# Kernel optimization log

Measured on AMD Instinct MI355X. Metric: run time of the kernel, lower is better.

Reference implementation:

```python
import jax, jax.numpy as jnp
import numpy as np

B, C, H, W = 2, 128, 64, 64
D_STATE = 16
EXPAND = 2
D_INNER = C * EXPAND          # 256
DT_RANK = -(-C // 16)         # 8
K = 4                         # scan directions
COMPRESS = 3
SQUEEZE = 30
EPS = 1e-5


def layernorm(x, g, b):
    mu = x.mean(-1, keepdims=True)
    xm = x - mu
    var = (xm * xm).mean(-1, keepdims=True)
    return xm * jax.lax.rsqrt(var + EPS) * g + b


def conv2d(x, w, bias, pad):
    y = jax.lax.conv_general_dilated(x, w, (1, 1), ((pad, pad), (pad, pad)),
                                     dimension_numbers=('NCHW', 'OIHW', 'NCHW'))
    return y + bias[None, :, None, None]


def selective_scan(xs, dts, A, Bs, Cs):
    # xs,dts: (B,K,D,L); A: (K,D,N); Bs,Cs: (B,K,N,L)
    dt_t = jnp.moveaxis(dts, -1, 0)
    x_t = jnp.moveaxis(xs, -1, 0)
    B_t = jnp.moveaxis(Bs, -1, 0)
    C_t = jnp.moveaxis(Cs, -1, 0)
    h0 = jnp.zeros(xs.shape[:3] + (A.shape[-1],), xs.dtype)

    def step(h, inp):
        dt_l, x_l, b_l, c_l = inp          # (B,K,D),(B,K,D),(B,K,N),(B,K,N)
        dA = jnp.exp(dt_l[..., None] * A)  # (B,K,D,N)
        h = dA * h + (dt_l * x_l)[..., None] * b_l[:, :, None, :]
        y = jnp.einsum('bkdn,bkn->bkd', h, c_l)
        return h, y

    _, ys = jax.lax.scan(step, h0, (dt_t, x_t, B_t, C_t))
    return jnp.moveaxis(ys, 0, -1)  # (B,K,D,L)


def ss2d(x, p):  # x: (B,H,W,C) -> (B,H,W,C)
    xz = x @ p['in_proj_w'].T
    xc, z = jnp.split(xz, 2, axis=-1)
    xc = xc.transpose(0, 3, 1, 2)  # (B,D,H,W)
    xc = jax.lax.conv_general_dilated(xc, p['conv_w'], (1, 1), ((1, 1), (1, 1)),
                                      feature_group_count=D_INNER,
                                      dimension_numbers=('NCHW', 'OIHW', 'NCHW'))
    xc = jax.nn.silu(xc + p['conv_b'][None, :, None, None])
    b, d, h, w = xc.shape
    L = h * w
    x_hw = xc.reshape(b, d, L)
    x_wh = xc.transpose(0, 1, 3, 2).reshape(b, d, L)
    xs = jnp.stack([x_hw, x_wh, x_hw[..., ::-1], x_wh[..., ::-1]], axis=1)  # (B,4,D,L)
    x_dbl = jnp.einsum('bkdl,kcd->bkcl', xs, p['x_proj_w'])
    dtr, Bs, Cs = jnp.split(x_dbl, [DT_RANK, DT_RANK + D_STATE], axis=2)
    dts = jnp.einsum('bkrl,kdr->bkdl', dtr, p['dt_w'])
    dts = jax.nn.softplus(dts + p['dt_b'][None, :, :, None])
    A = -jnp.exp(p['A_logs']).reshape(K, d, D_STATE)
    ys = selective_scan(xs, dts, A, Bs, Cs)
    ys = ys + xs * p['Ds'].reshape(K, d)[None, :, :, None]
    inv = ys[:, 2:4][..., ::-1]  # undo flipped scans
    wh = lambda t: t.reshape(b, d, w, h).transpose(0, 1, 3, 2).reshape(b, d, L)
    y = ys[:, 0] + inv[:, 0] + wh(ys[:, 1]) + wh(inv[:, 1])
    y = y.transpose(0, 2, 1).reshape(b, h, w, d)
    y = layernorm(y, p['out_norm_g'], p['out_norm_b'])
    y = y * jax.nn.silu(z)
    return y @ p['out_proj_w'].T


def cab(x, p):  # x: (B,C,H,W)
    t = jax.nn.gelu(conv2d(x, p['cab_w1'], p['cab_b1'], 1), approximate=False)
    t = conv2d(t, p['cab_w2'], p['cab_b2'], 1)
    s = t.mean((2, 3), keepdims=True)
    s = jax.nn.relu(conv2d(s, p['ca_w1'], p['ca_b1'], 0))
    s = jax.nn.sigmoid(conv2d(s, p['ca_w2'], p['ca_b2'], 0))
    return t * s


def vss_block(input, p):
    inp = input.transpose(0, 2, 3, 1)  # (B,H,W,C)
    x = inp * p['skip_scale'] + ss2d(layernorm(inp, p['ln1_g'], p['ln1_b']), p)
    c = cab(layernorm(x, p['ln2_g'], p['ln2_b']).transpose(0, 3, 1, 2), p)
    x = x * p['skip_scale2'] + c.transpose(0, 2, 3, 1)
    return x.transpose(0, 3, 1, 2)


def setup_inputs() -> dict:
    key = jax.random.key(0)
    ks = jax.random.split(key, 16)
    rn = lambda i, shp, s=0.02: jax.random.normal(ks[i], shp, jnp.float32) * s
    return {
        'input': jax.random.normal(ks[0], (B, C, H, W), jnp.float32),
        'ln1_g': jnp.ones((C,), jnp.float32), 'ln1_b': jnp.zeros((C,), jnp.float32),
        'skip_scale': jnp.ones((C,), jnp.float32), 'skip_scale2': jnp.ones((C,), jnp.float32),
        'ln2_g': jnp.ones((C,), jnp.float32), 'ln2_b': jnp.zeros((C,), jnp.float32),
        'in_proj_w': rn(1, (2 * D_INNER, C)),
        'conv_w': rn(2, (D_INNER, 1, 3, 3), 0.1),
        'conv_b': jnp.zeros((D_INNER,), jnp.float32),
        'x_proj_w': rn(3, (K, DT_RANK + 2 * D_STATE, D_INNER)),
        'dt_w': rn(4, (K, D_INNER, DT_RANK), 0.1),
        'dt_b': rn(5, (K, D_INNER), 0.1),
        'A_logs': jnp.log(jnp.tile(jnp.arange(1, D_STATE + 1, dtype=jnp.float32), (K * D_INNER, 1))),
        'Ds': jnp.ones((K * D_INNER,), jnp.float32),
        'out_norm_g': jnp.ones((D_INNER,), jnp.float32), 'out_norm_b': jnp.zeros((D_INNER,), jnp.float32),
        'out_proj_w': rn(6, (C, D_INNER)),
        'cab_w1': rn(7, (C // COMPRESS, C, 3, 3), 0.05),
        'cab_b1': jnp.zeros((C // COMPRESS,), jnp.float32),
        'cab_w2': rn(8, (C, C // COMPRESS, 3, 3), 0.05),
        'cab_b2': jnp.zeros((C,), jnp.float32),
        'ca_w1': rn(9, (C // SQUEEZE, C, 1, 1), 0.05),
        'ca_b1': jnp.zeros((C // SQUEEZE,), jnp.float32),
        'ca_w2': rn(10, (C, C // SQUEEZE, 1, 1), 0.05),
        'ca_b2': jnp.zeros((C,), jnp.float32),
    }


def reference(input, ln1_g, ln1_b, skip_scale, skip_scale2, ln2_g, ln2_b,
              in_proj_w, conv_w, conv_b, x_proj_w, dt_w, dt_b, A_logs, Ds,
              out_norm_g, out_norm_b, out_proj_w,
              cab_w1, cab_b1, cab_w2, cab_b2, ca_w1, ca_b1, ca_w2, ca_b2):
    p = dict(ln1_g=ln1_g, ln1_b=ln1_b, skip_scale=skip_scale, skip_scale2=skip_scale2,
             ln2_g=ln2_g, ln2_b=ln2_b, in_proj_w=in_proj_w, conv_w=conv_w, conv_b=conv_b,
             x_proj_w=x_proj_w, dt_w=dt_w, dt_b=dt_b, A_logs=A_logs, Ds=Ds,
             out_norm_g=out_norm_g, out_norm_b=out_norm_b, out_proj_w=out_proj_w,
             cab_w1=cab_w1, cab_b1=cab_b1, cab_w2=cab_w2, cab_b2=cab_b2,
             ca_w1=ca_w1, ca_b1=ca_b1, ca_w2=ca_w2, ca_b2=ca_b2)
    return vss_block(input, p)
```

## Files before the change

kernel.cpp:

```cpp
#include <hip/hip_runtime.h>
#include <math.h>

#define BB 2
#define CC 128
#define HH 64
#define WW 64
#define LL 4096
#define DI 256
#define NS 16
#define KK 4
#define OC1 42

#define NC 256
#define CL 16

#define K3_POS 16
#define BCW 48

__device__ __forceinline__ float sigmoidf_(float x) { return 1.f / (1.f + __expf(-x)); }
__device__ __forceinline__ float siluf_(float x)    { return x * sigmoidf_(x); }

__device__ __forceinline__ int scan_pos(int k, int i) {
  if (k == 0) return i;
  if (k == 1) return ((i & 63) << 6) | (i >> 6);
  if (k == 2) return (LL - 1) - i;
  int j = (LL - 1) - i;
  return ((j & 63) << 6) | (j >> 6);
}

__global__ __launch_bounds__(256) void k1_ln_inproj(
    const float* __restrict__ inp, const float* __restrict__ g, const float* __restrict__ b,
    const float* __restrict__ wproj, float* __restrict__ xcin, float* __restrict__ zbuf) {
  __shared__ float sx[64][132];
  __shared__ float sw[128][68];
  __shared__ float smu[64], srs[64];
  const int tid = threadIdx.x;
  const int rt = blockIdx.x & 3;
  const int pt = blockIdx.x >> 2;
  const int bb = pt >> 6;
  const int pbase = (pt & 63) << 6;

  for (int idx = tid; idx < 64 * CC; idx += 256) {
    int c = idx >> 6, pl = idx & 63;
    sx[pl][c] = inp[((size_t)bb * CC + c) * LL + pbase + pl];
  }
  __syncthreads();
  {
    int pl = tid >> 2, j = tid & 3;
    float s = 0.f, s2 = 0.f;
    for (int c = j; c < CC; c += 4) { float v = sx[pl][c]; s += v; s2 += v * v; }
    s += __shfl_xor(s, 1); s2 += __shfl_xor(s2, 1);
    s += __shfl_xor(s, 2); s2 += __shfl_xor(s2, 2);
    if (j == 0) {
      float mu = s * (1.f / CC);
      smu[pl] = mu;
      srs[pl] = rsqrtf(s2 * (1.f / CC) - mu * mu + 1e-5f);
    }
  }
  __syncthreads();
  for (int idx = tid; idx < 64 * CC; idx += 256) {
    int c = idx & 127, pl = idx >> 7;
    sx[pl][c] = (sx[pl][c] - smu[pl]) * srs[pl] * g[c] + b[c];
  }

  const int pg = tid & 7, rg = tid >> 3;
  float acc[8][4];
#pragma unroll
  for (int j = 0; j < 8; j++)
#pragma unroll
    for (int q = 0; q < 4; q++) acc[j][q] = 0.f;

  for (int kc = 0; kc < CC; kc += 64) {
    __syncthreads();
    for (int idx = tid; idx < 128 * 64; idx += 256) {
      int cl = idx & 63, rl = idx >> 6;
      sw[rl][cl] = wproj[(size_t)(rt * 128 + rl) * CC + kc + cl];
    }
    __syncthreads();
#pragma unroll 4
    for (int i = 0; i < 16; i++) {
      const int k0 = kc + 4 * i, kl0 = 4 * i;
      float4 xv[8], wv[4];
#pragma unroll
      for (int j = 0; j < 8; j++) xv[j] = *(const float4*)&sx[pg + 8 * j][k0];
#pragma unroll
      for (int q = 0; q < 4; q++) wv[q] = *(const float4*)&sw[rg + 32 * q][kl0];
#pragma unroll
      for (int j = 0; j < 8; j++)
#pragma unroll
        for (int q = 0; q < 4; q++) {
          acc[j][q] += xv[j].x * wv[q].x + xv[j].y * wv[q].y
                     + xv[j].z * wv[q].z + xv[j].w * wv[q].w;
        }
    }
  }

  float* buf = (rt < 2) ? xcin : zbuf;
  const int drow = (rt & 1) * 128;
#pragma unroll
  for (int j = 0; j < 8; j++) {
    const int p = pbase + pg + 8 * j;
    float* dst = buf + ((size_t)bb * LL + p) * DI + drow;
#pragma unroll
    for (int q = 0; q < 4; q++) dst[rg + 32 * q] = acc[j][q];
  }
}

__global__ __launch_bounds__(256) void k2_dwconv(
    const float* __restrict__ xcin, const float* __restrict__ cw, const float* __restrict__ cb,
    float* __restrict__ xconv) {
  const int w0 = (blockIdx.x & 7) * 8;
  const int hh = (blockIdx.x >> 3) & 63;
  const int bb = blockIdx.x >> 9;
  const int d = threadIdx.x;

  float wv[9];
#pragma unroll
  for (int kk = 0; kk < 9; kk++) wv[kk] = cw[d * 9 + kk];
  const float bias = cb[d];

  float xin[3][10];
#pragma unroll
  for (int kh = 0; kh < 3; kh++) {
    int r = hh + kh - 1;
    bool vr = (r >= 0 && r < HH);
#pragma unroll
    for (int c = 0; c < 10; c++) {
      int cc2 = w0 + c - 1;
      bool vc = (cc2 >= 0 && cc2 < WW);
      xin[kh][c] = (vr && vc) ? xcin[((size_t)bb * LL + r * WW + cc2) * DI + d] : 0.f;
    }
  }
#pragma unroll
  for (int j = 0; j < 8; j++) {
    float acc = bias;
#pragma unroll
    for (int kh = 0; kh < 3; kh++)
#pragma unroll
      for (int kw = 0; kw < 3; kw++)
        acc += wv[kh * 3 + kw] * xin[kh][j + kw];
    xconv[((size_t)bb * LL + hh * WW + w0 + j) * DI + d] = siluf_(acc);
  }
}

__global__ __launch_bounds__(256) void k3_proj(
    const float* __restrict__ xconv, const float* __restrict__ xpw,
    float* __restrict__ BCbuf) {
  __shared__ float sx[16][68];
  __shared__ float sw[160][68];
  const int tid = threadIdx.x;
  const int bb = blockIdx.x >> 8;
  const int pbase = (blockIdx.x & 255) << 4;

  const int pg = tid & 7, rb = tid >> 3;
  float acc[2][5];
#pragma unroll
  for (int j = 0; j < 2; j++)
#pragma unroll
    for (int q = 0; q < 5; q++) acc[j][q] = 0.f;

  for (int kc = 0; kc < DI; kc += 64) {
    __syncthreads();
    for (int idx = tid; idx < 16 * 64; idx += 256) {
      int cl = idx & 63, pl = idx >> 6;
      sx[pl][cl] = xconv[((size_t)bb * LL + pbase + pl) * DI + kc + cl];
    }
    for (int idx = tid; idx < 160 * 64; idx += 256) {
      int cl = idx & 63, rl = idx >> 6;
      sw[rl][cl] = xpw[(size_t)rl * DI + kc + cl];
    }
    __syncthreads();
#pragma unroll 4
    for (int i = 0; i < 16; i++) {
      float4 xv[2], wv[5];
#pragma unroll
      for (int j = 0; j < 2; j++) xv[j] = *(const float4*)&sx[2 * pg + j][4 * i];
#pragma unroll
      for (int q = 0; q < 5; q++) wv[q] = *(const float4*)&sw[rb + 32 * q][4 * i];
#pragma unroll
      for (int j = 0; j < 2; j++)
#pragma unroll
        for (int q = 0; q < 5; q++) {
          acc[j][q] += xv[j].x * wv[q].x + xv[j].y * wv[q].y
                     + xv[j].z * wv[q].z + xv[j].w * wv[q].w;
        }
    }
  }

#pragma unroll
  for (int j = 0; j < 2; j++) {
    const int p = pbase + 2 * pg + j;
#pragma unroll
    for (int q = 0; q < 5; q++) {
      const int r = rb + 32 * q;
      const int k = r / 40, c0 = r - k * 40;
      BCbuf[((size_t)(bb * KK + k) * LL + p) * BCW + c0] = acc[j][q];
    }
  }
}

__global__ __launch_bounds__(256) void k4a_chunk(
    const float* __restrict__ xconv, const float* __restrict__ BCbuf,
    const float* __restrict__ A_logs, const float* __restrict__ dtw,
    const float* __restrict__ dtb,
    float* __restrict__ csS, float* __restrict__ csB) {
  __shared__ float sBC[CL][26];
  const int d = threadIdx.x;
  const int chunk = blockIdx.x & (NC - 1);
  const int t = blockIdx.x / NC;
  const int k = t & 3;
  const int bb = t >> 2;
  const int bk = bb * KK + k;
  const int base = chunk * CL;

  for (int idx = d; idx < CL * 24; idx += 256) {
    int ii = idx / 24, j = idx - ii * 24;
    int pos = scan_pos(k, base + ii);
    sBC[ii][j] = BCbuf[((size_t)bk * LL + pos) * BCW + j];
  }
  float a[NS];
  bool fast = true;
#pragma unroll
  for (int n = 0; n < NS; n++) {
    a[n] = -__expf(A_logs[((size_t)k * DI + d) * NS + n]);
    fast = fast && (fabsf(a[n] + (float)(n + 1)) < 1e-3f * (n + 1));
  }
  const float* wdt = dtw + ((size_t)k * DI + d) * 8;
  const float4 wd0 = *(const float4*)wdt;
  const float4 wd1 = *(const float4*)(wdt + 4);
  const float bdt = dtb[k * DI + d];
  __syncthreads();

  const float* x_p = xconv + (size_t)bb * LL * DI + d;

  float Bc[NS];
#pragma unroll
  for (int n = 0; n < NS; n++) Bc[n] = 0.f;
  float sumdt = 0.f;

  if (fast) {
#pragma unroll
    for (int half = 0; half < CL / 8; half++) {
      float xvr[8];
#pragma unroll
      for (int j = 0; j < 8; j++)
        xvr[j] = x_p[(size_t)scan_pos(k, base + half * 8 + j) * DI];
#pragma unroll
      for (int j = 0; j < 8; j++) {
        const int ii = half * 8 + j;
        const float* dr = sBC[ii];
        float u = bdt + wd0.x * dr[0] + wd0.y * dr[1] + wd0.z * dr[2] + wd0.w * dr[3]
                      + wd1.x * dr[4] + wd1.y * dr[5] + wd1.z * dr[6] + wd1.w * dr[7];
        float t2 = __expf(u);
        float E = __builtin_amdgcn_rcpf(1.f + t2);
        float dt = u > 20.f ? u : -0.69314718056f * __log2f(E);
        sumdt += dt;
        float dtx = dt * xvr[j];
        float E2 = E * E;
        float dA1 = E, dA2 = E2;
#pragma unroll
        for (int n = 0; n < NS; n += 2) {
          Bc[n] = dA1 * Bc[n] + dtx * sBC[ii][8 + n];
          Bc[n + 1] = dA2 * Bc[n + 1] + dtx * sBC[ii][9 + n];
          dA1 *= E2; dA2 *= E2;
        }
      }
    }
  } else {
#pragma unroll 2
    for (int ii = 0; ii < CL; ii++) {
      int pos = scan_pos(k, base + ii);
      float xv = x_p[(size_t)pos * DI];
      const float* dr = sBC[ii];
      float u = bdt + wd0.x * dr[0] + wd0.y * dr[1] + wd0.z * dr[2] + wd0.w * dr[3]
                    + wd1.x * dr[4] + wd1.y * dr[5] + wd1.z * dr[6] + wd1.w * dr[7];
      float t2 = __expf(u);
      float dt = u > 20.f ? u : log1pf(t2);
      sumdt += dt;
      float dtx = dt * xv;
#pragma unroll
      for (int n = 0; n < NS; n++) {
        float dA = __expf(dt * a[n]);
        Bc[n] = dA * Bc[n] + dtx * sBC[ii][8 + n];
      }
    }
  }
  csS[((size_t)bk * NC + chunk) * DI + d] = sumdt;
  size_t e = ((size_t)(bk * NC + chunk) * NS) * DI + d;
#pragma unroll
  for (int n = 0; n < NS; n++)
    csB[e + (size_t)n * DI] = Bc[n];
}

__global__ __launch_bounds__(256) void k4b_scanchunks(
    const float* __restrict__ csS, const float* __restrict__ csB,
    const float* __restrict__ A_logs, float* __restrict__ hin) {
  const int d = threadIdx.x;
  const int n = blockIdx.x & (NS - 1);
  const int bk = blockIdx.x >> 4;
  const int k = bk & 3;
  const float an = -__expf(A_logs[((size_t)k * DI + d) * NS + n]);
  const size_t strideB = (size_t)NS * DI;
  size_t e = ((size_t)bk * NC * NS + n) * DI + d;
  float H = 0.f;
  for (int c0 = 0; c0 < NC; c0 += 16) {
    float Ea[16], Bv[16];
#pragma unroll
    for (int j = 0; j < 16; j++) {
      Ea[j] = an * csS[((size_t)bk * NC + c0 + j) * DI + d];
      Bv[j] = csB[e + (size_t)j * strideB];
    }
#pragma unroll
    for (int j = 0; j < 16; j++) Ea[j] = __expf(Ea[j]);
#pragma unroll
    for (int j = 0; j < 16; j++) {
      hin[e + (size_t)j * strideB] = H;
      H = Ea[j] * H + Bv[j];
    }
    e += (size_t)16 * strideB;
  }
}

__global__ __launch_bounds__(256) void k4c_scan(
    const float* __restrict__ xconv, const float* __restrict__ BCbuf,
    const float* __restrict__ A_logs, const float* __restrict__ dtw,
    const float* __restrict__ dtb, const float* __restrict__ Ds,
    const float* __restrict__ hin, float* __restrict__ ys) {
  __shared__ float sBC[CL][BCW];
  const int d = threadIdx.x;
  const int chunk = blockIdx.x & (NC - 1);
  const int t = blockIdx.x / NC;
  const int k = t & 3;
  const int bb = t >> 2;
  const int bk = bb * KK + k;
  const int base = chunk * CL;

  for (int idx = d; idx < CL * 40; idx += 256) {
    int ii = idx / 40, j = idx - ii * 40;
    int pos = scan_pos(k, base + ii);
    sBC[ii][j] = BCbuf[((size_t)bk * LL + pos) * BCW + j];
  }
  float a[NS], h[NS];
  bool fast = true;
  const size_t eh = ((size_t)(bk * NC + chunk) * NS) * DI + d;
#pragma unroll
  for (int n = 0; n < NS; n++) {
    a[n] = -__expf(A_logs[((size_t)k * DI + d) * NS + n]);
    fast = fast && (fabsf(a[n] + (float)(n + 1)) < 1e-3f * (n + 1));
    h[n] = hin[eh + (size_t)n * DI];
  }
  const float* wdt = dtw + ((size_t)k * DI + d) * 8;
  const float4 wd0 = *(const float4*)wdt;
  const float4 wd1 = *(const float4*)(wdt + 4);
  const float bdt = dtb[k * DI + d];
  const float Dd = Ds[k * DI + d];
  __syncthreads();

  const float* x_p = xconv + (size_t)bb * LL * DI + d;
  float* ys_p = ys + (size_t)bk * LL * DI + d;

  if (fast) {
#pragma unroll
    for (int half = 0; half < CL / 8; half++) {
      float xvr[8];
#pragma unroll
      for (int j = 0; j < 8; j++)
        xvr[j] = x_p[(size_t)scan_pos(k, base + half * 8 + j) * DI];
#pragma unroll
      for (int j = 0; j < 8; j++) {
        const int ii = half * 8 + j;
        const float* dr = sBC[ii];
        float u = bdt + wd0.x * dr[0] + wd0.y * dr[1] + wd0.z * dr[2] + wd0.w * dr[3]
                      + wd1.x * dr[4] + wd1.y * dr[5] + wd1.z * dr[6] + wd1.w * dr[7];
        float t2 = __expf(u);
        float E = __builtin_amdgcn_rcpf(1.f + t2);
        float dt = u > 20.f ? u : -0.69314718056f * __log2f(E);
        float dtx = dt * xvr[j];
        float y = xvr[j] * Dd;
        float E2 = E * E;
        float dA1 = E, dA2 = E2;
#pragma unroll
        for (int n = 0; n < NS; n += 2) {
          h[n] = dA1 * h[n] + dtx * sBC[ii][8 + n];
          y += h[n] * sBC[ii][24 + n];
          h[n + 1] = dA2 * h[n + 1] + dtx * sBC[ii][9 + n];
          y += h[n + 1] * sBC[ii][25 + n];
          dA1 *= E2; dA2 *= E2;
        }
        ys_p[(size_t)scan_pos(k, base + ii) * DI] = y;
      }
    }
  } else {
#pragma unroll 2
    for (int ii = 0; ii < CL; ii++) {
      int pos = scan_pos(k, base + ii);
      float xv = x_p[(size_t)pos * DI];
      const float* dr = sBC[ii];
      float u = bdt + wd0.x * dr[0] + wd0.y * dr[1] + wd0.z * dr[2] + wd0.w * dr[3]
                    + wd1.x * dr[4] + wd1.y * dr[5] + wd1.z * dr[6] + wd1.w * dr[7];
      float t2 = __expf(u);
      float dt = u > 20.f ? u : log1pf(t2);
      float dtx = dt * xv;
      float y = xv * Dd;
#pragma unroll
      for (int n = 0; n < NS; n++) {
        float dA = __expf(dt * a[n]);
        h[n] = dA * h[n] + dtx * sBC[ii][8 + n];
        y += h[n] * sBC[ii][24 + n];
      }
      ys_p[(size_t)pos * DI] = y;
    }
  }
}

__global__ __launch_bounds__(256) void k5_fused(
    const float* __restrict__ ys, const float* __restrict__ zbuf,
    const float* __restrict__ ong, const float* __restrict__ onb,
    const float* __restrict__ opw,
    const float* __restrict__ inp, const float* __restrict__ sk,
    const float* __restrict__ g2, const float* __restrict__ b2,
    float* __restrict__ xresT, float* __restrict__ ln2) {
  __shared__ float sy[16][260];
  __shared__ float sw[128][68];
  __shared__ float sr[16][132];
  __shared__ float smu[16], srs[16];
  const int tid = threadIdx.x;
  const int bb = blockIdx.x >> 8;
  const int pbase = (blockIdx.x & 255) << 4;

  for (int idx = tid; idx < 16 * DI; idx += 256) {
    int d = idx & 255, pl = idx >> 8;
    size_t o0 = (((size_t)bb * KK + 0) * LL + pbase + pl) * DI + d;
    const size_t st = (size_t)LL * DI;
    sy[pl][d] = ys[o0] + ys[o0 + st] + ys[o0 + 2 * st] + ys[o0 + 3 * st];
  }
  __syncthreads();
  {
    int pl = tid >> 4, j = tid & 15;
    float s = 0.f, s2 = 0.f;
    for (int d = j; d < DI; d += 16) { float v = sy[pl][d]; s += v; s2 += v * v; }
#pragma unroll
    for (int m = 1; m < 16; m <<= 1) { s += __shfl_xor(s, m); s2 += __shfl_xor(s2, m); }
    if (j == 0) {
      float mu = s * (1.f / DI);
      smu[pl] = mu;
      srs[pl] = rsqrtf(s2 * (1.f / DI) - mu * mu + 1e-5f);
    }
  }
  __syncthreads();
  for (int idx = tid; idx < 16 * DI; idx += 256) {
    int d = idx & 255, pl = idx >> 8;
    float zv = zbuf[((size_t)bb * LL + pbase + pl) * DI + d];
    sy[pl][d] = ((sy[pl][d] - smu[pl]) * srs[pl] * ong[d] + onb[d]) * siluf_(zv);
  }

  const int pg = tid & 7, rb = tid >> 3;
  float acc[2][4];
#pragma unroll
  for (int j = 0; j < 2; j++)
#pragma unroll
    for (int q = 0; q < 4; q++) acc[j][q] = 0.f;

  for (int kc = 0; kc < DI; kc += 64) {
    __syncthreads();
    for (int idx = tid; idx < 128 * 64; idx += 256) {
      int cl = idx & 63, rl = idx >> 6;
      sw[rl][cl] = opw[(size_t)rl * DI + kc + cl];
    }
    __syncthreads();
#pragma unroll 4
    for (int i = 0; i < 16; i++) {
      float4 xv[2], wv[4];
#pragma unroll
      for (int j = 0; j < 2; j++) xv[j] = *(const float4*)&sy[2 * pg + j][kc + 4 * i];
#pragma unroll
      for (int q = 0; q < 4; q++) wv[q] = *(const float4*)&sw[rb + 32 * q][4 * i];
#pragma unroll
      for (int j = 0; j < 2; j++)
#pragma unroll
        for (int q = 0; q < 4; q++) {
          acc[j][q] += xv[j].x * wv[q].x + xv[j].y * wv[q].y
                     + xv[j].z * wv[q].z + xv[j].w * wv[q].w;
        }
    }
  }

#pragma unroll
  for (int j = 0; j < 2; j++) {
    const int p = pbase + 2 * pg + j;
#pragma unroll
    for (int q = 0; q < 4; q++) {
      const int c = rb + 32 * q;
      float r = inp[((size_t)bb * CC + c) * LL + p] * sk[c] + acc[j][q];
      sr[2 * pg + j][c] = r;
    }
  }
  __syncthreads();
  {
    int pl = tid >> 4, jj = tid & 15;
    float s = 0.f, s2 = 0.f;
    for (int c = jj; c < CC; c += 16) { float v = sr[pl][c]; s += v; s2 += v * v; }
#pragma unroll
    for (int m = 1; m < 16; m <<= 1) { s += __shfl_xor(s, m); s2 += __shfl_xor(s2, m); }
    if (jj == 0) {
      float mu = s * (1.f / CC);
      smu[pl] = mu;
      srs[pl] = rsqrtf(s2 * (1.f / CC) - mu * mu + 1e-5f);
    }
  }
  __syncthreads();
  for (int idx = tid; idx < 16 * CC; idx += 256) {
    int pl = idx & 15, c = idx >> 4;
    float r = sr[pl][c];
    size_t o = ((size_t)bb * CC + c) * LL + pbase + pl;
    xresT[o] = r;
    ln2[o] = (r - smu[pl]) * srs[pl] * g2[c] + b2[c];
  }
}

__global__ __launch_bounds__(256) void k6a_conv1(
    const float* __restrict__ ln2, const float* __restrict__ w1,
    float* __restrict__ pc1) {
  __shared__ float sIn[16][6][68];
  __shared__ float sw[16 * 9 * OC1];
  const int tid = threadIdx.x;
  const int icq = blockIdx.x & 7;
  const int h4  = (blockIdx.x >> 3) & 15;
  const int bb  = blockIdx.x >> 7;
  const int icb = icq * 16;

  for (int idx = tid; idx < 16 * 6 * 66; idx += 256) {
    int i = idx / 396, rem = idx % 396;
    int rr = rem / 66, j = rem % 66;
    int r = h4 * 4 + rr - 1, c2 = j - 1;
    float v = 0.f;
    if (r >= 0 && r < HH && c2 >= 0 && c2 < WW)
      v = ln2[((size_t)bb * CC + icb + i) * LL + r * WW + c2];
    sIn[i][rr][j] = v;
  }
  for (int idx = tid; idx < OC1 * 16 * 9; idx += 256) {
    int oc = idx / 144, rem = idx % 144;
    int i = rem / 9, kk = rem % 9;
    sw[(i * 9 + kk) * OC1 + oc] = w1[((size_t)oc * CC + icb + i) * 9 + kk];
  }
  __syncthreads();

  const int wq = tid & 7, hq = (tid >> 3) & 3, ocg = tid >> 5;
  float acc[6][8];
#pragma unroll
  for (int q = 0; q < 6; q++)
#pragma unroll
    for (int ww = 0; ww < 8; ww++) acc[q][ww] = 0.f;

  for (int i = 0; i < 16; i++) {
    float xin[3][10];
#pragma unroll
    for (int kh = 0; kh < 3; kh++)
#pragma unroll
      for (int j = 0; j < 10; j++) xin[kh][j] = sIn[i][hq + kh][wq * 8 + j];
#pragma unroll
    for (int q = 0; q < 6; q++) {
      int oc = ocg + 8 * q;
      if (oc >= OC1) break;
      float wv[9];
#pragma unroll
      for (int kk = 0; kk < 9; kk++) wv[kk] = sw[(i * 9 + kk) * OC1 + oc];
#pragma unroll
      for (int kh = 0; kh < 3; kh++)
#pragma unroll
        for (int kw = 0; kw < 3; kw++)
#pragma unroll
          for (int ww = 0; ww < 8; ww++)
            acc[q][ww] += wv[kh * 3 + kw] * xin[kh][ww + kw];
    }
  }

  const int hrow = h4 * 4 + hq;
#pragma unroll
  for (int q = 0; q < 6; q++) {
    int oc = ocg + 8 * q;
    if (oc >= OC1) break;
    float* dst = pc1 + (((size_t)icq * BB + bb) * OC1 + oc) * LL + hrow * WW + wq * 8;
    *(float4*)dst       = make_float4(acc[q][0], acc[q][1], acc[q][2], acc[q][3]);
    *(float4*)(dst + 4) = make_float4(acc[q][4], acc[q][5], acc[q][6], acc[q][7]);
  }
}

__global__ __launch_bounds__(256) void k6b_reduce(
    const float* __restrict__ pc1, const float* __restrict__ b1,
    float* __restrict__ t1) {
  const int oc = blockIdx.x % OC1;
  const int bb = blockIdx.x / OC1;
  const float bias = b1[oc];
  const size_t st = (size_t)BB * OC1 * LL;
  const float* src = pc1 + ((size_t)bb * OC1 + oc) * LL;
  float* dst = t1 + ((size_t)bb * OC1 + oc) * LL;
  for (int i = threadIdx.x; i < LL / 4; i += 256) {
    float4 s = ((const float4*)src)[i];
#pragma unroll
    for (int icq = 1; icq < 8; icq++) {
      float4 v = *(const float4*)(src + (size_t)icq * st + i * 4);
      s.x += v.x; s.y += v.y; s.z += v.z; s.w += v.w;
    }
    float r[4] = {s.x + bias, s.y + bias, s.z + bias, s.w + bias};
#pragma unroll
    for (int q = 0; q < 4; q++)
      r[q] = 0.5f * r[q] * (1.f + erff(r[q] * 0.70710678118654752f));
    ((float4*)dst)[i] = make_float4(r[0], r[1], r[2], r[3]);
  }
}

__global__ __launch_bounds__(256) void k7_conv2(
    const float* __restrict__ t1, const float* __restrict__ w2,
    float* __restrict__ pc2) {
  __shared__ float sIn[21][4][68];
  __shared__ float swT[32 * 196];
  const int tid = threadIdx.x;
  const int icq = blockIdx.x & 1;
  const int h2  = (blockIdx.x >> 1) & 31;
  const int ocq = (blockIdx.x >> 6) & 3;
  const int bb  = blockIdx.x >> 8;
  const int icb = icq * 21;

  for (int idx = tid; idx < 21 * 4 * 66; idx += 256) {
    int i = idx / 264, rem = idx % 264;
    int rr = rem / 66, j = rem % 66;
    int r = h2 * 2 + rr - 1, c2 = j - 1;
    float v = 0.f;
    if (r >= 0 && r < HH && c2 >= 0 && c2 < WW)
      v = t1[((size_t)bb * OC1 + icb + i) * LL + r * WW + c2];
    sIn[i][rr][j] = v;
  }
  for (int idx = tid; idx < 32 * 189; idx += 256) {
    int ol = idx / 189, ikk = idx % 189;
    swT[ol * 196 + ikk] = w2[(size_t)(ocq * 32 + ol) * (OC1 * 9) + icb * 9 + ikk];
  }
  __syncthreads();

  const int wq = tid & 7, hq = (tid >> 3) & 1, ocg = tid >> 4;
  float acc[2][8];
#pragma unroll
  for (int q = 0; q < 2; q++)
#pragma unroll
    for (int ww = 0; ww < 8; ww++) acc[q][ww] = 0.f;

  for (int i = 0; i < 21; i++) {
    float xin[3][10];
#pragma unroll
    for (int kh = 0; kh < 3; kh++)
#pragma unroll
      for (int j = 0; j < 10; j++) xin[kh][j] = sIn[i][hq + kh][wq * 8 + j];
#pragma unroll
    for (int q = 0; q < 2; q++) {
      int ol = ocg + 16 * q;
      float wv[9];
#pragma unroll
      for (int kk = 0; kk < 9; kk++) wv[kk] = swT[ol * 196 + i * 9 + kk];
#pragma unroll
      for (int kh = 0; kh < 3; kh++)
#pragma unroll
        for (int kw = 0; kw < 3; kw++)
#pragma unroll
          for (int ww = 0; ww < 8; ww++)
            acc[q][ww] += wv[kh * 3 + kw] * xin[kh][ww + kw];
    }
  }

  const int hrow = h2 * 2 + hq;
#pragma unroll
  for (int q = 0; q < 2; q++) {
    int oc = ocq * 32 + ocg + 16 * q;
    float* dst = pc2 + (((size_t)icq * BB + bb) * CC + oc) * LL + hrow * WW + wq * 8;
    *(float4*)dst       = make_float4(acc[q][0], acc[q][1], acc[q][2], acc[q][3]);
    *(float4*)(dst + 4) = make_float4(acc[q][4], acc[q][5], acc[q][6], acc[q][7]);
  }
}

__global__ __launch_bounds__(256) void k8_mean(
    const float* __restrict__ pc2, const float* __restrict__ b2,
    float* __restrict__ t2, float* __restrict__ smean) {
  __shared__ float red[4];
  const int bc = blockIdx.x;
  const int bb = bc >> 7, c = bc & 127;
  const float bias = b2[c];
  const size_t st = (size_t)BB * CC * LL;
  const float* src = pc2 + ((size_t)bb * CC + c) * LL;
  float* dst = t2 + (size_t)bc * LL;
  float s = 0.f;
  for (int i = threadIdx.x; i < LL / 4; i += 256) {
    float4 v0 = ((const float4*)src)[i];
    float4 v1 = *(const float4*)(src + st + i * 4);
    float4 r = make_float4(v0.x + v1.x + bias, v0.y + v1.y + bias,
                           v0.z + v1.z + bias, v0.w + v1.w + bias);
    ((float4*)dst)[i] = r;
    s += r.x + r.y + r.z + r.w;
  }
#pragma unroll
  for (int m = 1; m < 64; m <<= 1) s += __shfl_xor(s, m);
  if ((threadIdx.x & 63) == 0) red[threadIdx.x >> 6] = s;
  __syncthreads();
  if (threadIdx.x == 0) smean[bc] = (red[0] + red[1] + red[2] + red[3]) * (1.f / LL);
}

__global__ __launch_bounds__(256) void k10_final(
    const float* __restrict__ xresT, const float* __restrict__ t2,
    const float* __restrict__ smean,
    const float* __restrict__ cw1, const float* __restrict__ cb1,
    const float* __restrict__ cw2, const float* __restrict__ cb2,
    const float* __restrict__ sk2, float* __restrict__ out) {
  __shared__ float mid[4];
  const int tid = threadIdx.x;
  const int bc = blockIdx.x;
  const int bb = bc >> 7, c = bc & 127;

  {
    const int wv = tid >> 6, ln = tid & 63;
    float s = cw1[wv * CC + ln] * smean[bb * CC + ln]
            + cw1[wv * CC + 64 + ln] * smean[bb * CC + 64 + ln];
#pragma unroll
    for (int m = 1; m < 64; m <<= 1) s += __shfl_xor(s, m);
    if (ln == 0) mid[wv] = fmaxf(s + cb1[wv], 0.f);
  }
  __syncthreads();
  float a = cb2[c];
#pragma unroll
  for (int m = 0; m < 4; m++) a += cw2[c * 4 + m] * mid[m];
  const float sv = sigmoidf_(a);

  const float ss = sk2[c];
  const float* t2r = t2 + (size_t)bc * LL;
  const float* xrt = xresT + (size_t)bc * LL;
  float* outr = out + (size_t)bc * LL;
  for (int i = tid; i < LL; i += 256)
    outr[i] = xrt[i] * ss + t2r[i] * sv;
}


extern "C" void kernel_launch(void* const* d_in, const int* in_sizes, int n_in,
                              void* d_out, int out_size, void* d_ws, size_t ws_size,
                              hipStream_t stream) {
  const float* input      = (const float*)d_in[0];
  const float* ln1_g      = (const float*)d_in[1];
  const float* ln1_b      = (const float*)d_in[2];
  const float* skip_scale = (const float*)d_in[3];
  const float* skip_scale2= (const float*)d_in[4];
  const float* ln2_g      = (const float*)d_in[5];
  const float* ln2_b      = (const float*)d_in[6];
  const float* in_proj_w  = (const float*)d_in[7];
  const float* conv_w     = (const float*)d_in[8];
  const float* conv_b     = (const float*)d_in[9];
  const float* x_proj_w   = (const float*)d_in[10];
  const float* dt_w       = (const float*)d_in[11];
  const float* dt_b       = (const float*)d_in[12];
  const float* A_logs     = (const float*)d_in[13];
  const float* Ds         = (const float*)d_in[14];
  const float* out_norm_g = (const float*)d_in[15];
  const float* out_norm_b = (const float*)d_in[16];
  const float* out_proj_w = (const float*)d_in[17];
  const float* cab_w1     = (const float*)d_in[18];
  const float* cab_b1     = (const float*)d_in[19];
  const float* cab_w2     = (const float*)d_in[20];
  const float* cab_b2     = (const float*)d_in[21];
  const float* ca_w1      = (const float*)d_in[22];
  const float* ca_b1      = (const float*)d_in[23];
  const float* ca_w2      = (const float*)d_in[24];
  const float* ca_b2      = (const float*)d_in[25];

  float* ws = (float*)d_ws;
  float* xcin  = ws;
  float* zbuf  = xcin + (size_t)BB * LL * DI;
  float* xconv = zbuf + (size_t)BB * LL * DI;
  float* BCbuf = xconv + (size_t)BB * LL * DI;
  float* ysb   = BCbuf + (size_t)BB * KK * LL * BCW;
  float* xresT = ysb + (size_t)BB * KK * LL * DI;
  float* ln2b  = xresT + (size_t)BB * LL * CC;
  float* t1b   = ln2b + (size_t)BB * CC * LL;
  float* t2b   = t1b + (size_t)BB * OC1 * LL;
  float* smean = t2b + (size_t)BB * CC * LL;
  float* hinbuf= smean + BB * CC;
  float* csS   = hinbuf + (size_t)BB * KK * NC * NS * DI;
  float* csB   = ysb;
  float* pc1   = ysb;
  float* pc2   = ysb + (size_t)3 * 1024 * 1024;

  k1_ln_inproj<<<512, 256, 0, stream>>>(input, ln1_g, ln1_b, in_proj_w, xcin, zbuf);
  k2_dwconv<<<BB * HH * (WW / 8), 256, 0, stream>>>(xcin, conv_w, conv_b, xconv);
  k3_proj<<<BB * (LL / K3_POS), 256, 0, stream>>>(xconv, x_proj_w, BCbuf);
  k4a_chunk<<<BB * KK * NC, 256, 0, stream>>>(xconv, BCbuf, A_logs, dt_w, dt_b, csS, csB);
  k4b_scanchunks<<<BB * KK * NS, 256, 0, stream>>>(csS, csB, A_logs, hinbuf);
  k4c_scan<<<BB * KK * NC, 256, 0, stream>>>(xconv, BCbuf, A_logs, dt_w, dt_b, Ds, hinbuf, ysb);
  k5_fused<<<BB * (LL / 16), 256, 0, stream>>>(ysb, zbuf, out_norm_g, out_norm_b, out_proj_w,
                                               input, skip_scale, ln2_g, ln2_b, xresT, ln2b);
  k6a_conv1<<<BB * 16 * 8, 256, 0, stream>>>(ln2b, cab_w1, pc1);
  k6b_reduce<<<BB * OC1, 256, 0, stream>>>(pc1, cab_b1, t1b);
  k7_conv2<<<BB * 4 * 32 * 2, 256, 0, stream>>>(t1b, cab_w2, pc2);
  k8_mean<<<BB * CC, 256, 0, stream>>>(pc2, cab_b2, t2b, smean);
  k10_final<<<BB * CC, 256, 0, stream>>>(xresT, t2b, smean, ca_w1, ca_b1, ca_w2, ca_b2,
                                         skip_scale2, (float*)d_out);
}
```

Baseline: 242.7 us.

## Store z, chunk states, hidden inputs and scan outputs in bf16

Switches several large intermediate buffers (z gate, per-chunk B accumulators, chunk-entry hidden states, and the four-direction scan outputs) from fp32 to bf16 storage, with all arithmetic still in fp32. The goal is to roughly halve the memory traffic of the scan and fused output kernels, which are bandwidth-heavy. The cost is reduced precision in the stored hidden states and outputs, which could affect accuracy. Stores are 2-byte scalars that may coalesce less efficiently.

```diff
diff --git a/kernel.cpp b/kernel.cpp
--- a/kernel.cpp
+++ b/kernel.cpp
@@ -1,4 +1,5 @@
 #include <hip/hip_runtime.h>
+#include <hip/hip_bf16.h>
 #include <math.h>
 
 #define BB 2
@@ -17,6 +18,8 @@
 #define K3_POS 16
 #define BCW 48
 
+typedef __hip_bfloat16 bf16;
+
 __device__ __forceinline__ float sigmoidf_(float x) { return 1.f / (1.f + __expf(-x)); }
 __device__ __forceinline__ float siluf_(float x)    { return x * sigmoidf_(x); }
 
@@ -30,7 +33,7 @@
 
 __global__ __launch_bounds__(256) void k1_ln_inproj(
     const float* __restrict__ inp, const float* __restrict__ g, const float* __restrict__ b,
-    const float* __restrict__ wproj, float* __restrict__ xcin, float* __restrict__ zbuf) {
+    const float* __restrict__ wproj, float* __restrict__ xcin, bf16* __restrict__ zbuf) {
   __shared__ float sx[64][132];
   __shared__ float sw[128][68];
   __shared__ float smu[64], srs[64];
@@ -95,14 +98,18 @@
     }
   }
 
-  float* buf = (rt < 2) ? xcin : zbuf;
-  const int drow = (rt & 1) * 128;
 #pragma unroll
   for (int j = 0; j < 8; j++) {
     const int p = pbase + pg + 8 * j;
-    float* dst = buf + ((size_t)bb * LL + p) * DI + drow;
-#pragma unroll
-    for (int q = 0; q < 4; q++) dst[rg + 32 * q] = acc[j][q];
+    if (rt < 2) {
+      float* dst = xcin + ((size_t)bb * LL + p) * DI + rt * 128;
+#pragma unroll
+      for (int q = 0; q < 4; q++) dst[rg + 32 * q] = acc[j][q];
+    } else {
+      bf16* dst = zbuf + ((size_t)bb * LL + p) * DI + (rt - 2) * 128;
+#pragma unroll
+      for (int q = 0; q < 4; q++) dst[rg + 32 * q] = __float2bfloat16(acc[j][q]);
+    }
   }
 }
 
@@ -203,7 +210,7 @@
     const float* __restrict__ xconv, const float* __restrict__ BCbuf,
     const float* __restrict__ A_logs, const float* __restrict__ dtw,
     const float* __restrict__ dtb,
-    float* __restrict__ csS, float* __restrict__ csB) {
+    float* __restrict__ csS, bf16* __restrict__ csB) {
   __shared__ float sBC[CL][26];
   const int d = threadIdx.x;
   const int chunk = blockIdx.x & (NC - 1);
@@ -289,12 +296,12 @@
   size_t e = ((size_t)(bk * NC + chunk) * NS) * DI + d;
 #pragma unroll
   for (int n = 0; n < NS; n++)
-    csB[e + (size_t)n * DI] = Bc[n];
+    csB[e + (size_t)n * DI] = __float2bfloat16(Bc[n]);
 }
 
 __global__ __launch_bounds__(256) void k4b_scanchunks(
-    const float* __restrict__ csS, const float* __restrict__ csB,
-    const float* __restrict__ A_logs, float* __restrict__ hin) {
+    const float* __restrict__ csS, const bf16* __restrict__ csB,
+    const float* __restrict__ A_logs, bf16* __restrict__ hin) {
   const int d = threadIdx.x;
   const int n = blockIdx.x & (NS - 1);
   const int bk = blockIdx.x >> 4;
@@ -308,13 +315,13 @@
 #pragma unroll
     for (int j = 0; j < 16; j++) {
       Ea[j] = an * csS[((size_t)bk * NC + c0 + j) * DI + d];
-      Bv[j] = csB[e + (size_t)j * strideB];
+      Bv[j] = __bfloat162float(csB[e + (size_t)j * strideB]);
     }
 #pragma unroll
     for (int j = 0; j < 16; j++) Ea[j] = __expf(Ea[j]);
 #pragma unroll
     for (int j = 0; j < 16; j++) {
-      hin[e + (size_t)j * strideB] = H;
+      hin[e + (size_t)j * strideB] = __float2bfloat16(H);
       H = Ea[j] * H + Bv[j];
     }
     e += (size_t)16 * strideB;
@@ -325,7 +332,7 @@
     const float* __restrict__ xconv, const float* __restrict__ BCbuf,
     const float* __restrict__ A_logs, const float* __restrict__ dtw,
     const float* __restrict__ dtb, const float* __restrict__ Ds,
-    const float* __restrict__ hin, float* __restrict__ ys) {
+    const bf16* __restrict__ hin, bf16* __restrict__ ys) {
   __shared__ float sBC[CL][BCW];
   const int d = threadIdx.x;
   const int chunk = blockIdx.x & (NC - 1);
@@ -347,7 +354,7 @@
   for (int n = 0; n < NS; n++) {
     a[n] = -__expf(A_logs[((size_t)k * DI + d) * NS + n]);
     fast = fast && (fabsf(a[n] + (float)(n + 1)) < 1e-3f * (n + 1));
-    h[n] = hin[eh + (size_t)n * DI];
+    h[n] = __bfloat162float(hin[eh + (size_t)n * DI]);
   }
   const float* wdt = dtw + ((size_t)k * DI + d) * 8;
   const float4 wd0 = *(const float4*)wdt;
@@ -357,7 +364,7 @@
   __syncthreads();
 
   const float* x_p = xconv + (size_t)bb * LL * DI + d;
-  float* ys_p = ys + (size_t)bk * LL * DI + d;
+  bf16* ys_p = ys + (size_t)bk * LL * DI + d;
 
   if (fast) {
 #pragma unroll
@@ -387,7 +394,7 @@
           y += h[n + 1] * sBC[ii][25 + n];
           dA1 *= E2; dA2 *= E2;
         }
-        ys_p[(size_t)scan_pos(k, base + ii) * DI] = y;
+        ys_p[(size_t)scan_pos(k, base + ii) * DI] = __float2bfloat16(y);
       }
     }
   } else {
@@ -408,13 +415,13 @@
         h[n] = dA * h[n] + dtx * sBC[ii][8 + n];
         y += h[n] * sBC[ii][24 + n];
       }
-      ys_p[(size_t)pos * DI] = y;
+      ys_p[(size_t)pos * DI] = __float2bfloat16(y);
     }
   }
 }
 
 __global__ __launch_bounds__(256) void k5_fused(
-    const float* __restrict__ ys, const float* __restrict__ zbuf,
+    const bf16* __restrict__ ys, const bf16* __restrict__ zbuf,
     const float* __restrict__ ong, const float* __restrict__ onb,
     const float* __restrict__ opw,
     const float* __restrict__ inp, const float* __restrict__ sk,
@@ -432,7 +439,8 @@
     int d = idx & 255, pl = idx >> 8;
     size_t o0 = (((size_t)bb * KK + 0) * LL + pbase + pl) * DI + d;
     const size_t st = (size_t)LL * DI;
-    sy[pl][d] = ys[o0] + ys[o0 + st] + ys[o0 + 2 * st] + ys[o0 + 3 * st];
+    sy[pl][d] = __bfloat162float(ys[o0]) + __bfloat162float(ys[o0 + st])
+              + __bfloat162float(ys[o0 + 2 * st]) + __bfloat162float(ys[o0 + 3 * st]);
   }
   __syncthreads();
   {
@@ -450,7 +458,7 @@
   __syncthreads();
   for (int idx = tid; idx < 16 * DI; idx += 256) {
     int d = idx & 255, pl = idx >> 8;
-    float zv = zbuf[((size_t)bb * LL + pbase + pl) * DI + d];
+    float zv = __bfloat162float(zbuf[((size_t)bb * LL + pbase + pl) * DI + d]);
     sy[pl][d] = ((sy[pl][d] - smu[pl]) * srs[pl] * ong[d] + onb[d]) * siluf_(zv);
   }
 
@@ -768,28 +776,31 @@
 
   float* ws = (float*)d_ws;
   float* xcin  = ws;
-  float* zbuf  = xcin + (size_t)BB * LL * DI;
-  float* xconv = zbuf + (size_t)BB * LL * DI;
+  float* zb_f  = xcin + (size_t)BB * LL * DI;
+  bf16*  zbuf  = (bf16*)zb_f;
+  float* xconv = zb_f + (size_t)BB * LL * DI;
   float* BCbuf = xconv + (size_t)BB * LL * DI;
-  float* ysb   = BCbuf + (size_t)BB * KK * LL * BCW;
-  float* xresT = ysb + (size_t)BB * KK * LL * DI;
+  float* ysb_f = BCbuf + (size_t)BB * KK * LL * BCW;
+  float* xresT = ysb_f + (size_t)BB * KK * LL * DI;
   float* ln2b  = xresT + (size_t)BB * LL * CC;
   float* t1b   = ln2b + (size_t)BB * CC * LL;
   float* t2b   = t1b + (size_t)BB * OC1 * LL;
   float* smean = t2b + (size_t)BB * CC * LL;
-  float* hinbuf= smean + BB * CC;
-  float* csS   = hinbuf + (size_t)BB * KK * NC * NS * DI;
-  float* csB   = ysb;
-  float* pc1   = ysb;
-  float* pc2   = ysb + (size_t)3 * 1024 * 1024;
+  float* hin_f = smean + BB * CC;
+  bf16*  hinbuf= (bf16*)hin_f;
+  float* csS   = hin_f + (size_t)BB * KK * NC * NS * DI;
+  bf16*  csB   = (bf16*)ysb_f;
+  bf16*  ysbuf = (bf16*)ysb_f;
+  float* pc1   = ysb_f;
+  float* pc2   = ysb_f + (size_t)3 * 1024 * 1024;
 
   k1_ln_inproj<<<512, 256, 0, stream>>>(input, ln1_g, ln1_b, in_proj_w, xcin, zbuf);
   k2_dwconv<<<BB * HH * (WW / 8), 256, 0, stream>>>(xcin, conv_w, conv_b, xconv);
   k3_proj<<<BB * (LL / K3_POS), 256, 0, stream>>>(xconv, x_proj_w, BCbuf);
   k4a_chunk<<<BB * KK * NC, 256, 0, stream>>>(xconv, BCbuf, A_logs, dt_w, dt_b, csS, csB);
   k4b_scanchunks<<<BB * KK * NS, 256, 0, stream>>>(csS, csB, A_logs, hinbuf);
-  k4c_scan<<<BB * KK * NC, 256, 0, stream>>>(xconv, BCbuf, A_logs, dt_w, dt_b, Ds, hinbuf, ysb);
-  k5_fused<<<BB * (LL / 16), 256, 0, stream>>>(ysb, zbuf, out_norm_g, out_norm_b, out_proj_w,
+  k4c_scan<<<BB * KK * NC, 256, 0, stream>>>(xconv, BCbuf, A_logs, dt_w, dt_b, Ds, hinbuf, ysbuf);
+  k5_fused<<<BB * (LL / 16), 256, 0, stream>>>(ysbuf, zbuf, out_norm_g, out_norm_b, out_proj_w,
                                                input, skip_scale, ln2_g, ln2_b, xresT, ln2b);
   k6a_conv1<<<BB * 16 * 8, 256, 0, stream>>>(ln2b, cab_w1, pc1);
   k6b_reduce<<<BB * OC1, 256, 0, stream>>>(pc1, cab_b1, t1b);
```

Result: no change. 240.5 us, median of 3 (-0.9%).
